# Performance work log

Measured on AMD Instinct MI355X. Metric: run time of the kernel, lower is better.

The kernel has to match this reference:

```python
import jax, jax.numpy as jnp
import numpy as np

DT = 0.1
NUM_STEPS = 10
THRESHOLD = 0.3


def setup_inputs() -> dict:
    key = jax.random.key(0)
    k1, k2, k3 = jax.random.split(key, 3)
    B, T, D = 8, 4096, 1024
    L, O = 3, 4
    x = jax.random.normal(k1, (B, T, D), dtype=jnp.float32)
    # nn.Linear(dim, O, bias=False) weights per level, stacked: (L, O, D)
    W = jax.random.normal(k2, (L, O, D), dtype=jnp.float32) / np.sqrt(D)
    # omegas init: randn*0.1 + freq_scales[min(i,2)], freq_scales=[4.0,2.0,0.6]
    freq = jnp.array([4.0, 2.0, 0.6], dtype=jnp.float32)[:, None]
    omegas = jax.random.normal(k3, (L, O), dtype=jnp.float32) * 0.1 + freq
    # coupling strengths: 1.0 + i*0.5
    Ks = 1.0 + 0.5 * jnp.arange(L, dtype=jnp.float32)
    return {"x": x, "W": W, "omegas": omegas, "Ks": Ks}


def reference(x, W, omegas, Ks):
    B, T, D = x.shape
    L, O, _ = W.shape
    two_pi = 2.0 * jnp.pi

    # per-level projection: (L, B, T, O)
    proj = jnp.einsum('btd,lod->lbto', x, W)
    # initial phases from adjacent oscillator ratio
    phases = jnp.arctan2(proj, jnp.roll(proj, 1, axis=-1) + 1e-8) % two_pi

    om = omegas[:, None, None, :]      # (L,1,1,O)
    K = Ks[:, None, None, None]        # (L,1,1,1)

    def step(ph, _):
        # mean phase over time dim per oscillator (circular mean)
        mean_phase = jnp.arctan2(jnp.sin(ph).mean(axis=2, keepdims=True),
                                 jnp.cos(ph).mean(axis=2, keepdims=True))
        coupling = K * jnp.sin(mean_phase - ph) / T
        return (ph + DT * (om + coupling)) % two_pi, None

    phases, _ = jax.lax.scan(step, phases, None, length=NUM_STEPS)

    s = jnp.sin(phases)
    c = jnp.cos(phases)
    # global coherence: |mean_t exp(i*phi)| averaged over oscillators -> (B, L)
    level_coherences = jnp.sqrt(s.mean(axis=2) ** 2 + c.mean(axis=2) ** 2).mean(-1).T

    # sliding window-of-3 coherence along T -> (L, B, T-2)
    ms = (s[:, :, :-2] + s[:, :, 1:-1] + s[:, :, 2:]) / 3.0
    mc = (c[:, :, :-2] + c[:, :, 1:-1] + c[:, :, 2:]) / 3.0
    coh = jnp.sqrt(ms ** 2 + mc ** 2).mean(-1)
    # local-minimum dip detection: boundary at coherence index i+1 (i in 1..T-5)
    cond = (coh[..., 1:-1] < coh[..., :-2] - THRESHOLD) & \
           (coh[..., 1:-1] < coh[..., 2:] - THRESHOLD)      # (L, B, T-4)
    boundary_mask = jnp.pad(cond, ((0, 0), (0, 0), (2, 0)))   # (L, B, T-2)

    return phases, level_coherences, boundary_mask
```

## Files before the change

kernel.cpp:

```cpp
#include <hip/hip_runtime.h>
#include <math.h>

#define NB 8
#define NT 4096
#define ND 1024
#define NL 3
#define NO 4
#define NLO 12
#define TWO_PI_D 6.283185307179586476925286766559
#define DT_D 0.1
#define NSTEPS 10
#define THRESH_D 0.3

__global__ __launch_bounds__(256) void k_wprep(const float* __restrict__ W,
                                               double* __restrict__ wsW)
{
    int i = blockIdx.x * 256 + threadIdx.x;
    if (i < NLO * ND) wsW[i] = (double)W[i];
}

__global__ __launch_bounds__(512, 4) void k_proj(
    const float* __restrict__ x, const double* __restrict__ wsW,
    double* __restrict__ ws_ph, float* __restrict__ ws_s,
    float* __restrict__ ws_c)
{
    __shared__ char buf[65536];
    const int tid = threadIdx.x;
    const int lane = tid & 63;
    const int wid = __builtin_amdgcn_readfirstlane(tid >> 6);
    const long row0 = (long)blockIdx.x * 64;
    const double* wbase = wsW + wid * 128;
    float* tile = reinterpret_cast<float*>(buf) + wid * 2048;

    double acc[NLO];
#pragma unroll
    for (int lo = 0; lo < NLO; ++lo) acc[lo] = 0.0;

    const int rg = lane >> 3;
    const int slot = lane & 7;

    for (int it = 0; it < 4; ++it) {
#pragma unroll
        for (int p = 0; p < 8; ++p) {
            int r = p * 8 + rg;
            float4 v = *reinterpret_cast<const float4*>(
                x + (row0 + r) * ND + wid * 128 + it * 32 + slot * 4);
            *reinterpret_cast<float4*>(
                &tile[r * 32 + ((slot ^ (r & 7)) * 4)]) = v;
        }
        float4 f[8];
#pragma unroll
        for (int q = 0; q < 8; ++q)
            f[q] = *reinterpret_cast<const float4*>(
                &tile[lane * 32 + ((q ^ (lane & 7)) * 4)]);

        const double* wp = wbase + it * 32;
#pragma unroll
        for (int q = 0; q < 8; ++q) {
            double x0 = (double)f[q].x, x1 = (double)f[q].y;
            double x2 = (double)f[q].z, x3 = (double)f[q].w;
#pragma unroll
            for (int lo = 0; lo < NLO; ++lo) {
                double a = acc[lo];
                a = fma(x0, wp[lo * ND + q * 4 + 0], a);
                a = fma(x1, wp[lo * ND + q * 4 + 1], a);
                a = fma(x2, wp[lo * ND + q * 4 + 2], a);
                a = fma(x3, wp[lo * ND + q * 4 + 3], a);
                acc[lo] = a;
            }
        }
    }

    __syncthreads();
    double* red = reinterpret_cast<double*>(buf);
#pragma unroll
    for (int lo = 0; lo < NLO; ++lo)
        red[(wid * 64 + lane) * 13 + lo] = acc[lo];
    __syncthreads();

    if (tid < 192) {
        const int l = tid >> 6;
        const int rs = tid & 63;
        double proj[NO];
#pragma unroll
        for (int o = 0; o < NO; ++o) {
            int lo = l * NO + o;
            double p0 = 0.0;
#pragma unroll
            for (int w = 0; w < 8; ++w)
                p0 += red[(w * 64 + rs) * 13 + lo];
            proj[o] = p0;
        }
        const long r = row0 + rs;
        const int b = (int)(r >> 12);
        const int t = (int)(r & (NT - 1));
#pragma unroll
        for (int o = 0; o < NO; ++o) {
            double y = proj[o];
            double xx = proj[(o + 3) & 3] + 1e-8;
            double ph = atan2(y, xx);
            if (ph < 0.0) ph += TWO_PI_D;
            double r2 = sqrt(y * y + xx * xx);
            double s, cc;
            if (r2 > 0.0) { s = y / r2; cc = xx / r2; } else { s = 0.0; cc = 1.0; }
            long idx = ((long)((l * NB + b) * NO + o)) * NT + t;
            ws_ph[idx] = ph; ws_s[idx] = (float)s; ws_c[idx] = (float)cc;
        }
    }
}

#define B_THREADS 512
#define B_ELEMS (NT / B_THREADS)

__global__ __launch_bounds__(B_THREADS) void k_kuramoto(
    const float* __restrict__ omegas, const float* __restrict__ Ks,
    double* __restrict__ ws_ph, float* __restrict__ ws_s,
    float* __restrict__ ws_c, double* __restrict__ ws_r,
    float* __restrict__ out_ph)
{
    const int g = blockIdx.x;
    const int l = g >> 5;
    const int b = (g >> 2) & 7;
    const int o = g & 3;
    const double om = (double)omegas[l * NO + o];
    const double Kv = (double)Ks[l];
    const double dtom = DT_D * om;
    const double cKT = DT_D * Kv / (double)NT;
    double sA, cA; sincos(dtom, &sA, &cA);
    const int tid = threadIdx.x;
    const int wid = tid >> 6;
    const int lane = tid & 63;
    __shared__ double lds[18];

    double ph[B_ELEMS], s[B_ELEMS], c[B_ELEMS];
#pragma unroll
    for (int k = 0; k < B_ELEMS; ++k) {
        long idx = (long)g * NT + tid + k * B_THREADS;
        ph[k] = ws_ph[idx]; s[k] = (double)ws_s[idx]; c[k] = (double)ws_c[idx];
    }

    for (int step = 0; step < NSTEPS; ++step) {
        double ts = 0.0, tc = 0.0;
#pragma unroll
        for (int k = 0; k < B_ELEMS; ++k) { ts += s[k]; tc += c[k]; }
#pragma unroll
        for (int off = 32; off > 0; off >>= 1) {
            ts += __shfl_down(ts, off);
            tc += __shfl_down(tc, off);
        }
        if (lane == 0) { lds[wid] = ts; lds[8 + wid] = tc; }
        __syncthreads();
        if (tid == 0) {
            double S = 0.0, C = 0.0;
#pragma unroll
            for (int w = 0; w < 8; ++w) { S += lds[w]; C += lds[8 + w]; }
            double r2 = sqrt(S * S + C * C);
            double sm, cm;
            if (r2 > 0.0) { sm = S / r2; cm = C / r2; } else { sm = 0.0; cm = 1.0; }
            lds[16] = sm; lds[17] = cm;
        }
        __syncthreads();
        const double sm = lds[16], cm = lds[17];
#pragma unroll
        for (int k = 0; k < B_ELEMS; ++k) {
            double sv = sm * c[k] - cm * s[k];
            double eps = cKT * sv;
            double val = ph[k] + (dtom + eps);
            if (val >= TWO_PI_D) val -= TWO_PI_D;
            if (val < 0.0) val += TWO_PI_D;
            ph[k] = val;
            double sd = fma(cA, eps, sA);
            double cd = fma(-sA, eps, cA);
            double sn = fma(s[k], cd, c[k] * sd);
            double cn = fma(c[k], cd, -(s[k] * sd));
            s[k] = sn; c[k] = cn;
        }
        __syncthreads();
    }
    {
        double ts = 0.0, tc = 0.0;
#pragma unroll
        for (int k = 0; k < B_ELEMS; ++k) { ts += s[k]; tc += c[k]; }
#pragma unroll
        for (int off = 32; off > 0; off >>= 1) {
            ts += __shfl_down(ts, off);
            tc += __shfl_down(tc, off);
        }
        if (lane == 0) { lds[wid] = ts; lds[8 + wid] = tc; }
        __syncthreads();
        if (tid == 0) {
            double S = 0.0, C = 0.0;
#pragma unroll
            for (int w = 0; w < 8; ++w) { S += lds[w]; C += lds[8 + w]; }
            double Sm = S / (double)NT, Cm = C / (double)NT;
            ws_r[g] = sqrt(Sm * Sm + Cm * Cm);
        }
    }
#pragma unroll
    for (int k = 0; k < B_ELEMS; ++k) {
        int t = tid + k * B_THREADS;
        long idx = (long)g * NT + t;
        ws_s[idx] = (float)s[k]; ws_c[idx] = (float)c[k];
        out_ph[((long)(l * NB + b) * NT + t) * NO + o] = (float)ph[k];
    }
}

__global__ __launch_bounds__(256) void k_mask(
    const float* __restrict__ ws_s, const float* __restrict__ ws_c,
    float* __restrict__ out_mask)
{
    const int bid = blockIdx.x;
    const int lb = bid >> 4;
    const int t0 = ((bid & 15) << 8) + threadIdx.x;
    float* mrow = out_mask + (long)lb * (NT - 2);
    if ((bid & 15) == 0 && threadIdx.x < 2) mrow[threadIdx.x] = 0.0f;
    if (t0 >= NT - 4) return;
    double q[3] = {0.0, 0.0, 0.0};
#pragma unroll
    for (int o = 0; o < NO; ++o) {
        const float* ps = ws_s + ((long)lb * NO + o) * NT + t0;
        const float* pc = ws_c + ((long)lb * NO + o) * NT + t0;
        double sv[5], cv[5];
#pragma unroll
        for (int j = 0; j < 5; ++j) { sv[j] = (double)ps[j]; cv[j] = (double)pc[j]; }
#pragma unroll
        for (int j = 0; j < 3; ++j) {
            double ms = ((sv[j] + sv[j + 1]) + sv[j + 2]) / 3.0;
            double mc = ((cv[j] + cv[j + 1]) + cv[j + 2]) / 3.0;
            q[j] += sqrt(ms * ms + mc * mc);
        }
    }
    double coh0 = q[0] / 4.0, coh1 = q[1] / 4.0, coh2 = q[2] / 4.0;
    bool cond = (coh1 < coh0 - THRESH_D) && (coh1 < coh2 - THRESH_D);
    mrow[2 + t0] = cond ? 1.0f : 0.0f;
}

__global__ void k_level(const double* __restrict__ ws_r, float* __restrict__ out_lvl)
{
    const int tid = threadIdx.x;
    if (tid < NB * NL) {
        const int b = tid / NL, l = tid % NL;
        const double* r = ws_r + (long)(l * NB + b) * NO;
        double m = (((r[0] + r[1]) + r[2]) + r[3]) / 4.0;
        out_lvl[tid] = (float)m;
    }
}

extern "C" void kernel_launch(void* const* d_in, const int* in_sizes, int n_in,
                              void* d_out, int out_size, void* d_ws, size_t ws_size,
                              hipStream_t stream)
{
    const float* x      = (const float*)d_in[0];
    const float* W      = (const float*)d_in[1];
    const float* omegas = (const float*)d_in[2];
    const float* Ks     = (const float*)d_in[3];
    float* out = (float*)d_out;

    double* wsW   = (double*)d_ws;
    double* ws_ph = wsW + NLO * ND;
    float*  ws_s  = (float*)(ws_ph + (long)NLO * NB * NT);
    float*  ws_c  = ws_s + (long)NLO * NB * NT;
    double* ws_r  = (double*)(ws_c + (long)NLO * NB * NT);

    float* out_ph   = out;
    float* out_lvl  = out + 393216;
    float* out_mask = out + 393240;

    k_wprep<<<(NLO * ND + 255) / 256, 256, 0, stream>>>(W, wsW);
    k_proj<<<NB * NT / 64, 512, 0, stream>>>(x, wsW, ws_ph, ws_s, ws_c);
    k_kuramoto<<<NL * NB * NO, B_THREADS, 0, stream>>>(omegas, Ks, ws_ph, ws_s, ws_c, ws_r, out_ph);
    k_mask<<<24 * 16, 256, 0, stream>>>(ws_s, ws_c, out_mask);
    k_level<<<1, 64, 0, stream>>>(ws_r, out_lvl);
}
```

Baseline: 69.84 us.

## Double-buffer x tiles in LDS with register prefetch in projection kernel

Restructures the per-wave x tile loading in the projection kernel into 8 chunks of 16 columns, double-buffered in LDS. The next chunk's global loads are issued into registers before the current chunk's FMAs run, and stored to the alternate buffer afterward. This is meant to overlap global memory latency with the double-precision FMA work instead of stalling at each iteration. It raises register pressure from the prefetched float4s and converted doubles.

```diff
diff --git a/kernel.cpp b/kernel.cpp
--- a/kernel.cpp
+++ b/kernel.cpp
@@ -30,43 +30,71 @@
     const int wid = __builtin_amdgcn_readfirstlane(tid >> 6);
     const long row0 = (long)blockIdx.x * 64;
     const double* wbase = wsW + wid * 128;
-    float* tile = reinterpret_cast<float*>(buf) + wid * 2048;
+    char* tile = buf + wid * 8192;
+
+    const int rg = lane >> 2;
+    const int slot = lane & 3;
+    const float* xbase = x + row0 * ND + wid * 128;
 
     double acc[NLO];
 #pragma unroll
     for (int lo = 0; lo < NLO; ++lo) acc[lo] = 0.0;
 
-    const int rg = lane >> 3;
-    const int slot = lane & 7;
-
-    for (int it = 0; it < 4; ++it) {
-#pragma unroll
-        for (int p = 0; p < 8; ++p) {
-            int r = p * 8 + rg;
-            float4 v = *reinterpret_cast<const float4*>(
-                x + (row0 + r) * ND + wid * 128 + it * 32 + slot * 4);
-            *reinterpret_cast<float4*>(
-                &tile[r * 32 + ((slot ^ (r & 7)) * 4)]) = v;
-        }
-        float4 f[8];
-#pragma unroll
-        for (int q = 0; q < 8; ++q)
+    float4 fr[4];
+#pragma unroll
+    for (int p = 0; p < 4; ++p) {
+        int r = p * 16 + rg;
+        fr[p] = *reinterpret_cast<const float4*>(xbase + (long)r * ND + slot * 4);
+    }
+#pragma unroll
+    for (int p = 0; p < 4; ++p) {
+        int r = p * 16 + rg;
+        *reinterpret_cast<float4*>(tile + r * 64 + ((slot ^ (r & 3)) * 16)) = fr[p];
+    }
+
+#pragma unroll
+    for (int it = 0; it < 8; ++it) {
+        if (it < 7) {
+#pragma unroll
+            for (int p = 0; p < 4; ++p) {
+                int r = p * 16 + rg;
+                fr[p] = *reinterpret_cast<const float4*>(
+                    xbase + (long)r * ND + (it + 1) * 16 + slot * 4);
+            }
+        }
+        const char* th = tile + (it & 1) * 4096;
+        float4 f[4];
+#pragma unroll
+        for (int q = 0; q < 4; ++q)
             f[q] = *reinterpret_cast<const float4*>(
-                &tile[lane * 32 + ((q ^ (lane & 7)) * 4)]);
-
-        const double* wp = wbase + it * 32;
-#pragma unroll
-        for (int q = 0; q < 8; ++q) {
-            double x0 = (double)f[q].x, x1 = (double)f[q].y;
-            double x2 = (double)f[q].z, x3 = (double)f[q].w;
+                th + lane * 64 + ((q ^ (lane & 3)) * 16));
+        const double* wp = wbase + it * 16;
+        double xd[16];
+#pragma unroll
+        for (int q = 0; q < 4; ++q) {
+            xd[q * 4 + 0] = (double)f[q].x;
+            xd[q * 4 + 1] = (double)f[q].y;
+            xd[q * 4 + 2] = (double)f[q].z;
+            xd[q * 4 + 3] = (double)f[q].w;
+        }
+#pragma unroll
+        for (int dd = 0; dd < 16; dd += 4) {
 #pragma unroll
             for (int lo = 0; lo < NLO; ++lo) {
                 double a = acc[lo];
-                a = fma(x0, wp[lo * ND + q * 4 + 0], a);
-                a = fma(x1, wp[lo * ND + q * 4 + 1], a);
-                a = fma(x2, wp[lo * ND + q * 4 + 2], a);
-                a = fma(x3, wp[lo * ND + q * 4 + 3], a);
+                a = fma(xd[dd + 0], wp[lo * ND + dd + 0], a);
+                a = fma(xd[dd + 1], wp[lo * ND + dd + 1], a);
+                a = fma(xd[dd + 2], wp[lo * ND + dd + 2], a);
+                a = fma(xd[dd + 3], wp[lo * ND + dd + 3], a);
                 acc[lo] = a;
+            }
+        }
+        if (it < 7) {
+            char* tn = tile + ((it + 1) & 1) * 4096;
+#pragma unroll
+            for (int p = 0; p < 4; ++p) {
+                int r = p * 16 + rg;
+                *reinterpret_cast<float4*>(tn + r * 64 + ((slot ^ (r & 3)) * 16)) = fr[p];
             }
         }
     }
```

Measured after the change: 73.08 us. 1.05x slower.

## Compute projection with FP64 MFMA and move phase init into Kuramoto kernel

Applied to the files above, without the earlier changes.

Replaces the scalar double-precision FMA projection with the 16x16x4 f64 MFMA instruction. W is pre-transposed and zero-padded to 16 columns, and x and W tiles are staged through LDS. A probe kernel discovers the MFMA output lane mapping at runtime. The atan2, normalisation and phase computation move from the projection kernel into the Kuramoto kernel, which now reads raw projections. The per-step reduction is also computed redundantly by every thread, which removes one barrier per step. This trades extra launches and redundant per-thread work for much higher FP64 throughput in the memory-bound projection.

```diff
diff --git a/kernel.cpp b/kernel.cpp
--- a/kernel.cpp
+++ b/kernel.cpp
@@ -7,105 +7,87 @@
 #define NL 3
 #define NO 4
 #define NLO 12
+#define NROWS (NB * NT)
 #define TWO_PI_D 6.283185307179586476925286766559
 #define DT_D 0.1
 #define NSTEPS 10
 #define THRESH_D 0.3
 
+typedef double f64x4 __attribute__((ext_vector_type(4)));
+
 __global__ __launch_bounds__(256) void k_wprep(const float* __restrict__ W,
-                                               double* __restrict__ wsW)
+                                               double* __restrict__ wsWt)
 {
     int i = blockIdx.x * 256 + threadIdx.x;
-    if (i < NLO * ND) wsW[i] = (double)W[i];
-}
-
-__global__ __launch_bounds__(512, 4) void k_proj(
-    const float* __restrict__ x, const double* __restrict__ wsW,
-    double* __restrict__ ws_ph, float* __restrict__ ws_s,
-    float* __restrict__ ws_c)
-{
-    __shared__ char buf[65536];
+    if (i < 1024 * 16) {
+        int k = i >> 4, col = i & 15;
+        wsWt[i] = (col < NLO) ? (double)W[col * ND + k] : 0.0;
+    }
+}
+
+__global__ void k_probe(int* __restrict__ probe)
+{
+    const int l = threadIdx.x;
+    f64x4 z = {0.0, 0.0, 0.0, 0.0};
+    double v = (double)(l & 15);
+    f64x4 d1 = __builtin_amdgcn_mfma_f64_16x16x4f64(v, 1.0, z, 0, 0, 0);
+    f64x4 d2 = __builtin_amdgcn_mfma_f64_16x16x4f64(1.0, v, z, 0, 0, 0);
+#pragma unroll
+    for (int n = 0; n < 4; ++n) {
+        probe[(l * 4 + n) * 2 + 0] = (int)(d1[n] * 0.25 + 0.5);
+        probe[(l * 4 + n) * 2 + 1] = (int)(d2[n] * 0.25 + 0.5);
+    }
+}
+
+__global__ __launch_bounds__(256) void k_proj(
+    const float* __restrict__ x, const double* __restrict__ wsWt,
+    const int* __restrict__ probe, double* __restrict__ ws_proj)
+{
+    __shared__ float  xs[64 * 68];
+    __shared__ double wl[64 * 18];
     const int tid = threadIdx.x;
     const int lane = tid & 63;
-    const int wid = __builtin_amdgcn_readfirstlane(tid >> 6);
+    const int wid = tid >> 6;
     const long row0 = (long)blockIdx.x * 64;
-    const double* wbase = wsW + wid * 128;
-    float* tile = reinterpret_cast<float*>(buf) + wid * 2048;
-
-    double acc[NLO];
-#pragma unroll
-    for (int lo = 0; lo < NLO; ++lo) acc[lo] = 0.0;
-
-    const int rg = lane >> 3;
-    const int slot = lane & 7;
-
-    for (int it = 0; it < 4; ++it) {
-#pragma unroll
-        for (int p = 0; p < 8; ++p) {
-            int r = p * 8 + rg;
+
+    const int rg = tid >> 2;
+    const int slot = tid & 3;
+
+    f64x4 acc = {0.0, 0.0, 0.0, 0.0};
+
+    for (int c = 0; c < 16; ++c) {
+        if (c) __syncthreads();
+#pragma unroll
+        for (int j = 0; j < 4; ++j) {
             float4 v = *reinterpret_cast<const float4*>(
-                x + (row0 + r) * ND + wid * 128 + it * 32 + slot * 4);
-            *reinterpret_cast<float4*>(
-                &tile[r * 32 + ((slot ^ (r & 7)) * 4)]) = v;
-        }
-        float4 f[8];
-#pragma unroll
-        for (int q = 0; q < 8; ++q)
-            f[q] = *reinterpret_cast<const float4*>(
-                &tile[lane * 32 + ((q ^ (lane & 7)) * 4)]);
-
-        const double* wp = wbase + it * 32;
-#pragma unroll
-        for (int q = 0; q < 8; ++q) {
-            double x0 = (double)f[q].x, x1 = (double)f[q].y;
-            double x2 = (double)f[q].z, x3 = (double)f[q].w;
-#pragma unroll
-            for (int lo = 0; lo < NLO; ++lo) {
-                double a = acc[lo];
-                a = fma(x0, wp[lo * ND + q * 4 + 0], a);
-                a = fma(x1, wp[lo * ND + q * 4 + 1], a);
-                a = fma(x2, wp[lo * ND + q * 4 + 2], a);
-                a = fma(x3, wp[lo * ND + q * 4 + 3], a);
-                acc[lo] = a;
-            }
-        }
-    }
-
-    __syncthreads();
-    double* red = reinterpret_cast<double*>(buf);
-#pragma unroll
-    for (int lo = 0; lo < NLO; ++lo)
-        red[(wid * 64 + lane) * 13 + lo] = acc[lo];
-    __syncthreads();
-
-    if (tid < 192) {
-        const int l = tid >> 6;
-        const int rs = tid & 63;
-        double proj[NO];
-#pragma unroll
-        for (int o = 0; o < NO; ++o) {
-            int lo = l * NO + o;
-            double p0 = 0.0;
-#pragma unroll
-            for (int w = 0; w < 8; ++w)
-                p0 += red[(w * 64 + rs) * 13 + lo];
-            proj[o] = p0;
-        }
-        const long r = row0 + rs;
-        const int b = (int)(r >> 12);
-        const int t = (int)(r & (NT - 1));
-#pragma unroll
-        for (int o = 0; o < NO; ++o) {
-            double y = proj[o];
-            double xx = proj[(o + 3) & 3] + 1e-8;
-            double ph = atan2(y, xx);
-            if (ph < 0.0) ph += TWO_PI_D;
-            double r2 = sqrt(y * y + xx * xx);
-            double s, cc;
-            if (r2 > 0.0) { s = y / r2; cc = xx / r2; } else { s = 0.0; cc = 1.0; }
-            long idx = ((long)((l * NB + b) * NO + o)) * NT + t;
-            ws_ph[idx] = ph; ws_s[idx] = (float)s; ws_c[idx] = (float)cc;
-        }
+                x + (row0 + rg) * ND + c * 64 + (slot + 4 * j) * 4);
+            *reinterpret_cast<float4*>(&xs[rg * 68 + (slot + 4 * j) * 4]) = v;
+        }
+        const double* wtg = wsWt + (long)c * 64 * 16;
+#pragma unroll
+        for (int j = 0; j < 4; ++j) {
+            int idx = tid + j * 256;
+            wl[(idx >> 4) * 18 + (idx & 15)] = wtg[idx];
+        }
+        __syncthreads();
+
+        const float*  xrow = &xs[(wid * 16 + (lane & 15)) * 68 + (lane >> 4)];
+        const double* wrow = &wl[(lane >> 4) * 18 + (lane & 15)];
+#pragma unroll
+        for (int kc = 0; kc < 16; ++kc) {
+            double a = (double)xrow[kc * 4];
+            double b = wrow[kc * 4 * 18];
+            acc = __builtin_amdgcn_mfma_f64_16x16x4f64(a, b, acc, 0, 0, 0);
+        }
+    }
+
+    const int* pr = probe + lane * 8;
+#pragma unroll
+    for (int n = 0; n < 4; ++n) {
+        int i = pr[n * 2 + 0];
+        int j = pr[n * 2 + 1];
+        if (j < NLO)
+            ws_proj[(long)j * NROWS + row0 + wid * 16 + i] = acc[n];
     }
 }
 
@@ -114,7 +96,7 @@
 
 __global__ __launch_bounds__(B_THREADS) void k_kuramoto(
     const float* __restrict__ omegas, const float* __restrict__ Ks,
-    double* __restrict__ ws_ph, float* __restrict__ ws_s,
+    const double* __restrict__ ws_proj, float* __restrict__ ws_s,
     float* __restrict__ ws_c, double* __restrict__ ws_r,
     float* __restrict__ out_ph)
 {
@@ -130,13 +112,23 @@
     const int tid = threadIdx.x;
     const int wid = tid >> 6;
     const int lane = tid & 63;
-    __shared__ double lds[18];
+    __shared__ double lds[16];
+
+    const double* pA = ws_proj + (long)(l * NO + o) * NROWS + (long)b * NT;
+    const double* pB = ws_proj + (long)(l * NO + ((o + 3) & 3)) * NROWS + (long)b * NT;
 
     double ph[B_ELEMS], s[B_ELEMS], c[B_ELEMS];
 #pragma unroll
     for (int k = 0; k < B_ELEMS; ++k) {
-        long idx = (long)g * NT + tid + k * B_THREADS;
-        ph[k] = ws_ph[idx]; s[k] = (double)ws_s[idx]; c[k] = (double)ws_c[idx];
+        int t = tid + k * B_THREADS;
+        double y = pA[t];
+        double xx = pB[t] + 1e-8;
+        double p = atan2(y, xx);
+        if (p < 0.0) p += TWO_PI_D;
+        ph[k] = p;
+        double r2 = sqrt(y * y + xx * xx);
+        if (r2 > 0.0) { s[k] = y / r2; c[k] = xx / r2; }
+        else          { s[k] = 0.0;    c[k] = 1.0; }
     }
 
     for (int step = 0; step < NSTEPS; ++step) {
@@ -150,17 +142,12 @@
         }
         if (lane == 0) { lds[wid] = ts; lds[8 + wid] = tc; }
         __syncthreads();
-        if (tid == 0) {
-            double S = 0.0, C = 0.0;
-#pragma unroll
-            for (int w = 0; w < 8; ++w) { S += lds[w]; C += lds[8 + w]; }
-            double r2 = sqrt(S * S + C * C);
-            double sm, cm;
-            if (r2 > 0.0) { sm = S / r2; cm = C / r2; } else { sm = 0.0; cm = 1.0; }
-            lds[16] = sm; lds[17] = cm;
-        }
-        __syncthreads();
-        const double sm = lds[16], cm = lds[17];
+        double S = 0.0, C = 0.0;
+#pragma unroll
+        for (int w = 0; w < 8; ++w) { S += lds[w]; C += lds[8 + w]; }
+        double rr = sqrt(S * S + C * C);
+        double sm, cm;
+        if (rr > 0.0) { sm = S / rr; cm = C / rr; } else { sm = 0.0; cm = 1.0; }
 #pragma unroll
         for (int k = 0; k < B_ELEMS; ++k) {
             double sv = sm * c[k] - cm * s[k];
@@ -256,19 +243,21 @@
     const float* Ks     = (const float*)d_in[3];
     float* out = (float*)d_out;
 
-    double* wsW   = (double*)d_ws;
-    double* ws_ph = wsW + NLO * ND;
-    float*  ws_s  = (float*)(ws_ph + (long)NLO * NB * NT);
-    float*  ws_c  = ws_s + (long)NLO * NB * NT;
-    double* ws_r  = (double*)(ws_c + (long)NLO * NB * NT);
+    double* wsWt    = (double*)d_ws;
+    double* ws_proj = wsWt + 1024 * 16;
+    float*  ws_s    = (float*)(ws_proj + (long)NLO * NROWS);
+    float*  ws_c    = ws_s + (long)NLO * NB * NT;
+    double* ws_r    = (double*)(ws_c + (long)NLO * NB * NT);
+    int*    probe   = (int*)(ws_r + 96);
 
     float* out_ph   = out;
     float* out_lvl  = out + 393216;
     float* out_mask = out + 393240;
 
-    k_wprep<<<(NLO * ND + 255) / 256, 256, 0, stream>>>(W, wsW);
-    k_proj<<<NB * NT / 64, 512, 0, stream>>>(x, wsW, ws_ph, ws_s, ws_c);
-    k_kuramoto<<<NL * NB * NO, B_THREADS, 0, stream>>>(omegas, Ks, ws_ph, ws_s, ws_c, ws_r, out_ph);
+    k_wprep<<<64, 256, 0, stream>>>(W, wsWt);
+    k_probe<<<1, 64, 0, stream>>>(probe);
+    k_proj<<<NROWS / 64, 256, 0, stream>>>(x, wsWt, probe, ws_proj);
+    k_kuramoto<<<NL * NB * NO, B_THREADS, 0, stream>>>(omegas, Ks, ws_proj, ws_s, ws_c, ws_r, out_ph);
     k_mask<<<24 * 16, 256, 0, stream>>>(ws_s, ws_c, out_mask);
     k_level<<<1, 64, 0, stream>>>(ws_r, out_lvl);
 }
```

Result: slower. 72.30 us (+3.5%).
